# Kernel optimization log

Measured on AMD Instinct MI355X. Metric: run time of the kernel, lower is better.

Reference implementation:

```python
import jax, jax.numpy as jnp
import numpy as np

N, E, D_IN, D_H, D_OUT = 100000, 1600000, 128, 128, 16


def setup_inputs() -> dict:
    key = jax.random.key(0)
    k_x, k_e, k_w1, k_w2 = jax.random.split(key, 4)
    x = jax.random.normal(k_x, (N, D_IN), dtype=jnp.float32)
    edge_index = jax.random.randint(k_e, (2, E), 0, N, dtype=jnp.int64)
    # glorot-ish init for the two GCNConv weight matrices
    W1 = jax.random.normal(k_w1, (D_IN, D_H), dtype=jnp.float32) * (1.0 / np.sqrt(D_IN))
    b1 = jnp.zeros((D_H,), dtype=jnp.float32)
    W2 = jax.random.normal(k_w2, (D_H, D_OUT), dtype=jnp.float32) * (1.0 / np.sqrt(D_H))
    b2 = jnp.zeros((D_OUT,), dtype=jnp.float32)
    return {"x": x, "edge_index": edge_index, "W1": W1, "b1": b1, "W2": W2, "b2": b2}


def _gcn_conv(x, src, dst, norm, W, b, n):
    # linear transform, gather from source nodes, normalize, scatter-add to targets
    h = x @ W                                   # [N, d_out]
    msg = h[src] * norm[:, None]                # [E+N, d_out]
    return jax.ops.segment_sum(msg, dst, num_segments=n) + b


def reference(x, edge_index, W1, b1, W2, b2):
    n = x.shape[0]
    # GCNConv default: add self-loops, symmetric normalization D^-1/2 A D^-1/2
    loops = jnp.arange(n, dtype=edge_index.dtype)
    src = jnp.concatenate([edge_index[0], loops])
    dst = jnp.concatenate([edge_index[1], loops])
    deg = jax.ops.segment_sum(jnp.ones_like(dst, dtype=x.dtype), dst, num_segments=n)
    dinv = jnp.where(deg > 0, jax.lax.rsqrt(deg), 0.0)
    norm = dinv[src] * dinv[dst]                # [E+N]

    h = _gcn_conv(x, src, dst, norm, W1, b1, n)
    h = jax.nn.relu(h)
    # dropout is identity in eval mode (reference uses eval / deterministic path)
    out = _gcn_conv(h, src, dst, norm, W2, b2, n)
    return out
```

## Files before the change

### kernel.cpp

```cpp
#include <hip/hip_runtime.h>

typedef unsigned int uint;
typedef __attribute__((ext_vector_type(8))) short bf16x8;
typedef __attribute__((ext_vector_type(4))) float f32x4;

#define D_IN 128
#define D_H  128
#define D_OUT 16
#define NPC 512
#define NPCSH 9
#define CLDS 224
#define P1 256
#define CAP 96
#define EBCAP 12288
#define WT_STRIDE 68
#define XL_STRIDE 68

static __device__ __forceinline__ float bflo(uint u) { return __uint_as_float(u << 16); }
static __device__ __forceinline__ float bfhi(uint u) { return __uint_as_float(u & 0xFFFF0000u); }
static __device__ __forceinline__ uint f2bf(float f) {
    uint b = __float_as_uint(f);
    return (b + 0x7FFFu + ((b >> 16) & 1u)) >> 16;
}
static __device__ __forceinline__ uint pk(float a, float b) {
    return f2bf(a) | (f2bf(b) << 16);
}


__global__ __launch_bounds__(256) void k_wpack(const float* __restrict__ W1,
                                               uint* __restrict__ Wp) {
    int p = blockIdx.x * 256 + threadIdx.x;
    int k2 = p >> 7, f = p & 127;
    Wp[p] = pk(W1[(size_t)(2 * k2) * 128 + f], W1[(size_t)(2 * k2 + 1) * 128 + f]);
}


__global__ __launch_bounds__(256) void k_fill2(const int* __restrict__ src,
                                               const int* __restrict__ dst, int E, int N, int C,
                                               int chunk, int* __restrict__ cnt1,
                                               uint* __restrict__ binned1) {
    __shared__ int cur[CLDS];
    int t = threadIdx.x, b = blockIdx.x;
    for (int i = t; i < C; i += 256) cur[i] = 0;
    __syncthreads();
    int e0 = b * chunk, e1 = min(e0 + chunk, E);
    for (int e = e0 + t; e < e1; e += 256) {
        int d = dst[e];
        d = max(0, min(d, N - 1));
        int s = src[e];
        s = max(0, min(s, N - 1));
        int c = d >> NPCSH;
        int p = atomicAdd(&cur[c], 1);
        if (p < CAP) binned1[((size_t)b * C + c) * CAP + p] = ((uint)(d & (NPC - 1)) << 17) | (uint)s;
    }
    __syncthreads();
    for (int i = t; i < C; i += 256) cnt1[(size_t)i * P1 + b] = min(cur[i], CAP);
}


__global__ __launch_bounds__(256) void k_p2(const uint* __restrict__ binned1,
                                            const int* __restrict__ cnt1, int N, int C,
                                            int* __restrict__ ssrc, int* __restrict__ rowptr,
                                            int* __restrict__ deg, float* __restrict__ dinv) {
    __shared__ uint eb[EBCAP];
    __shared__ int bcnt[P1], boff[P1], ncnt[NPC], nbase_[NPC], sdata[256];
    __shared__ int total_s;
    int c = blockIdx.x, t = threadIdx.x;
    int v = cnt1[(size_t)c * P1 + t];
    bcnt[t] = v;
    sdata[t] = v;
    __syncthreads();
    for (int off = 1; off < 256; off <<= 1) {
        int xv = (t >= off) ? sdata[t - off] : 0;
        __syncthreads();
        sdata[t] += xv;
        __syncthreads();
    }
    boff[t] = sdata[t] - v;
    if (t == 255) total_s = min(sdata[255], EBCAP);
    __syncthreads();
    int total = total_s;
    int w = t >> 6, lane = t & 63;
    for (int b = w; b < P1; b += 4) {
        int n = bcnt[b], o = boff[b];
        const uint* gp = binned1 + ((size_t)b * C + c) * CAP;
        for (int j = lane; j < n; j += 64)
            if (o + j < EBCAP) eb[o + j] = gp[j];
    }
    for (int i = t; i < NPC; i += 256) ncnt[i] = 0;
    __syncthreads();
    for (int j = t; j < total; j += 256) atomicAdd(&ncnt[eb[j] >> 17], 1);
    __syncthreads();
    int v0 = ncnt[2 * t], v1 = ncnt[2 * t + 1];
    int s2 = v0 + v1;
    sdata[t] = s2;
    __syncthreads();
    for (int off = 1; off < 256; off <<= 1) {
        int xv = (t >= off) ? sdata[t - off] : 0;
        __syncthreads();
        sdata[t] += xv;
        __syncthreads();
    }
    int pre = sdata[t] - s2;
    nbase_[2 * t] = pre;
    nbase_[2 * t + 1] = pre + v0;
    __syncthreads();
    int rbase = c * EBCAP;
    for (int i = t; i < NPC; i += 256) {
        int node = c * NPC + i;
        if (node < N) {
            deg[node] = ncnt[i];
            rowptr[node] = rbase + nbase_[i];
            dinv[node] = rsqrtf((float)ncnt[i] + 1.0f);
        }
    }
    __syncthreads();
    for (int i = t; i < NPC; i += 256) ncnt[i] = nbase_[i];
    __syncthreads();
    for (int j = t; j < total; j += 256) {
        uint pe = eb[j];
        int p = atomicAdd(&ncnt[pe >> 17], 1);
        ssrc[rbase + p] = (int)(pe & 0x1FFFFu);
    }
}


__global__ __launch_bounds__(256) void k_gemm1(const float* __restrict__ x,
                                               const uint* __restrict__ Wp,
                                               const float* __restrict__ dinv, int N,
                                               uint* __restrict__ hs_b) {
    __shared__ uint Wt[128 * WT_STRIDE];
    __shared__ uint xl[128 * XL_STRIDE];
    int t = threadIdx.x;
    int row0 = blockIdx.x * 128;
    for (int p = t; p < 64 * 128; p += 256) {
        int k2 = p >> 7, f = p & 127;
        Wt[f * WT_STRIDE + k2] = Wp[p];
    }
    const float2* x2 = (const float2*)x;
    for (int p = t; p < 128 * 64; p += 256) {
        int r = p >> 6, cc = p & 63;
        int gr = row0 + r;
        float2 vv = (gr < N) ? x2[(size_t)gr * 64 + cc] : make_float2(0.f, 0.f);
        xl[r * XL_STRIDE + cc] = pk(vv.x, vv.y);
    }
    __syncthreads();
    int w = t >> 6, lane = t & 63;
    int q = lane >> 4, m = lane & 15;
    f32x4 acc[2][8];
#pragma unroll
    for (int ct = 0; ct < 2; ct++)
#pragma unroll
        for (int rt = 0; rt < 8; rt++) acc[ct][rt] = (f32x4){0.f, 0.f, 0.f, 0.f};
    for (int kc = 0; kc < 4; kc++) {
        bf16x8 afr[8];
#pragma unroll
        for (int rt = 0; rt < 8; rt++)
            afr[rt] = *(const bf16x8*)&xl[(rt * 16 + m) * XL_STRIDE + kc * 16 + q * 4];
#pragma unroll
        for (int ct = 0; ct < 2; ct++) {
            int f = w * 32 + ct * 16 + m;
            bf16x8 bfr = *(const bf16x8*)&Wt[f * WT_STRIDE + kc * 16 + q * 4];
#pragma unroll
            for (int rt = 0; rt < 8; rt++)
                acc[ct][rt] =
                    __builtin_amdgcn_mfma_f32_16x16x32_bf16(afr[rt], bfr, acc[ct][rt], 0, 0, 0);
        }
    }
    __syncthreads();
    uint* outl = xl;
#pragma unroll
    for (int rt = 0; rt < 8; rt++) {
        int gb = row0 + rt * 16 + q * 4;
        float4 dv;
        if (gb + 3 < N) {
            dv = *(const float4*)&dinv[gb];
        } else {
            dv.x = (gb < N) ? dinv[gb] : 0.f;
            dv.y = (gb + 1 < N) ? dinv[gb + 1] : 0.f;
            dv.z = (gb + 2 < N) ? dinv[gb + 2] : 0.f;
            dv.w = (gb + 3 < N) ? dinv[gb + 3] : 0.f;
        }
        float dr[4] = {dv.x, dv.y, dv.z, dv.w};
#pragma unroll
        for (int ct = 0; ct < 2; ct++) {
            f32x4 a = acc[ct][rt];
#pragma unroll
            for (int r = 0; r < 4; r++) {
                float vv = a[r] * dr[r];
                float vn = __shfl_xor(vv, 1);
                if (!(lane & 1)) {
                    int row = rt * 16 + q * 4 + r;
                    int cp = (w * 32 + ct * 16 + m) >> 1;
                    outl[row * 65 + cp] = pk(vv, vn);
                }
            }
        }
    }
    __syncthreads();
    for (int p = t; p < 128 * 64; p += 256) {
        int r = p >> 6, cc = p & 63;
        int gr = row0 + r;
        if (gr < N) hs_b[(size_t)gr * 64 + cc] = outl[r * 65 + cc];
    }
}


__global__ __launch_bounds__(256) void k_agg1(const uint* __restrict__ hs_b,
                                              const int* __restrict__ rowptr,
                                              const int* __restrict__ deg,
                                              const int* __restrict__ ssrc,
                                              const float* __restrict__ dinv,
                                              const float2* __restrict__ b1, int N,
                                              uint* __restrict__ rh_b) {
    int w = threadIdx.x >> 6, lane = threadIdx.x & 63;
    int d = blockIdx.x * 4 + w;
    if (d >= N) return;
    int start = rowptr[d], cnt = deg[d];
    uint sv = hs_b[((uint)d << 6) + lane];
    float a0 = bflo(sv), a1 = bfhi(sv);
    const int* sp = ssrc + start;
    int j = 0;
    for (; j + 8 <= cnt; j += 8) {
        int i0 = sp[j], i1 = sp[j + 1], i2 = sp[j + 2], i3 = sp[j + 3];
        int i4 = sp[j + 4], i5 = sp[j + 5], i6 = sp[j + 6], i7 = sp[j + 7];
        uint u0 = hs_b[((uint)i0 << 6) + lane];
        uint u1 = hs_b[((uint)i1 << 6) + lane];
        uint u2 = hs_b[((uint)i2 << 6) + lane];
        uint u3 = hs_b[((uint)i3 << 6) + lane];
        uint u4 = hs_b[((uint)i4 << 6) + lane];
        uint u5 = hs_b[((uint)i5 << 6) + lane];
        uint u6 = hs_b[((uint)i6 << 6) + lane];
        uint u7 = hs_b[((uint)i7 << 6) + lane];
        a0 += bflo(u0) + bflo(u1) + bflo(u2) + bflo(u3) + bflo(u4) + bflo(u5) + bflo(u6) +
              bflo(u7);
        a1 += bfhi(u0) + bfhi(u1) + bfhi(u2) + bfhi(u3) + bfhi(u4) + bfhi(u5) + bfhi(u6) +
              bfhi(u7);
    }
    for (; j < cnt; j++) {
        uint u = hs_b[((uint)sp[j] << 6) + lane];
        a0 += bflo(u);
        a1 += bfhi(u);
    }
    float sc = dinv[d];
    float2 bb = b1[lane];
    rh_b[((uint)d << 6) + lane] =
        pk(fmaxf(fmaf(a0, sc, bb.x), 0.f), fmaxf(fmaf(a1, sc, bb.y), 0.f));
}


__global__ __launch_bounds__(256) void k_gemm2(const uint* __restrict__ rh_b,
                                               const float* __restrict__ W2,
                                               const float* __restrict__ dinv, int N,
                                               uint* __restrict__ h2_b) {
    __shared__ float Wl[D_H * D_OUT];
    int t = threadIdx.x;
    for (int i = t; i < D_H * D_OUT; i += 256) Wl[i] = W2[i];
    __syncthreads();
    int r = blockIdx.x * 256 + t;
    if (r >= N) return;
    const uint* xrow = rh_b + (size_t)r * 64;
    float acc[16];
#pragma unroll
    for (int f = 0; f < 16; f++) acc[f] = 0.f;
    for (int c = 0; c < 16; c++) {
        uint4 xv = *(const uint4*)(xrow + c * 4);
        uint xs[4] = {xv.x, xv.y, xv.z, xv.w};
#pragma unroll
        for (int u = 0; u < 4; u++) {
            int k = c * 8 + u * 2;
            float x0 = bflo(xs[u]), x1 = bfhi(xs[u]);
            const float* w0 = &Wl[k * 16];
            const float* w1 = &Wl[(k + 1) * 16];
#pragma unroll
            for (int f = 0; f < 16; f++) acc[f] = fmaf(x0, w0[f], acc[f]);
#pragma unroll
            for (int f = 0; f < 16; f++) acc[f] = fmaf(x1, w1[f], acc[f]);
        }
    }
    float sc = dinv[r];
    uint o[8];
#pragma unroll
    for (int q = 0; q < 8; q++) o[q] = pk(acc[2 * q] * sc, acc[2 * q + 1] * sc);
    *(uint4*)&h2_b[(size_t)r * 8] = make_uint4(o[0], o[1], o[2], o[3]);
    *(uint4*)&h2_b[(size_t)r * 8 + 4] = make_uint4(o[4], o[5], o[6], o[7]);
}


__global__ __launch_bounds__(256) void k_agg2(const uint* __restrict__ h2_b,
                                              const int* __restrict__ rowptr,
                                              const int* __restrict__ deg,
                                              const int* __restrict__ ssrc,
                                              const float* __restrict__ dinv,
                                              const float* __restrict__ b2, int N,
                                              float2* __restrict__ out) {
    int w = threadIdx.x >> 6, lane = threadIdx.x & 63;
    int d = blockIdx.x * 4 + w;
    if (d >= N) return;
    int slot = lane >> 3, jp = lane & 7;
    int start = rowptr[d], cnt = deg[d];
    float a0 = 0.f, a1 = 0.f;
    if (slot == 0) {
        uint sv = h2_b[((uint)d << 3) + jp];
        a0 = bflo(sv);
        a1 = bfhi(sv);
    }
    const int* sp = ssrc + start;
    for (int j = slot; j < cnt; j += 8) {
        uint hv = h2_b[((uint)sp[j] << 3) + jp];
        a0 += bflo(hv);
        a1 += bfhi(hv);
    }
    a0 += __shfl_xor(a0, 8);
    a1 += __shfl_xor(a1, 8);
    a0 += __shfl_xor(a0, 16);
    a1 += __shfl_xor(a1, 16);
    a0 += __shfl_xor(a0, 32);
    a1 += __shfl_xor(a1, 32);
    if (slot == 0) {
        float di = dinv[d];
        out[(size_t)d * 8 + jp] =
            make_float2(fmaf(a0, di, b2[2 * jp]), fmaf(a1, di, b2[2 * jp + 1]));
    }
}


extern "C" void kernel_launch(void* const* d_in, const int* in_sizes, int n_in,
                              void* d_out, int out_size, void* d_ws, size_t ws_size,
                              hipStream_t stream) {
    const float* x  = (const float*)d_in[0];
    const int*   ei = (const int*)d_in[1];
    const float* W1 = (const float*)d_in[2];
    const float* b1 = (const float*)d_in[3];
    const float* W2 = (const float*)d_in[4];
    const float* b2 = (const float*)d_in[5];
    int N = in_sizes[0] / D_IN;
    int E = in_sizes[1] / 2;
    const int* src = ei;
    const int* dst = ei + E;
    int C = (N + NPC - 1) >> NPCSH;
    int chunk = (E + P1 - 1) / P1;

    char* ws = (char*)d_ws;
    size_t off = 0;
    auto alloc = [&](size_t bytes) -> char* {
        char* p = ws + off;
        off = (off + bytes + 255) & ~(size_t)255;
        return p;
    };
    uint*  Wp      = (uint*)alloc(8192 * 4);
    int*   cnt1    = (int*)alloc((size_t)P1 * C * 4);
    uint*  binned1 = (uint*)alloc((size_t)P1 * C * CAP * 4);
    int*   ssrc    = (int*)alloc((size_t)C * EBCAP * 4);
    int*   rowptr  = (int*)alloc((size_t)N * 4);
    int*   deg     = (int*)alloc((size_t)N * 4);
    float* dinv    = (float*)alloc((size_t)N * 4);
    uint*  hs_b    = (uint*)alloc((size_t)N * 64 * 4);
    uint*  rh_b    = (uint*)alloc((size_t)N * 64 * 4);
    uint*  h2_b    = hs_b;

    k_wpack<<<32, 256, 0, stream>>>(W1, Wp);
    k_fill2<<<P1, 256, 0, stream>>>(src, dst, E, N, C, chunk, cnt1, binned1);
    k_p2<<<C, 256, 0, stream>>>(binned1, cnt1, N, C, ssrc, rowptr, deg, dinv);
    k_gemm1<<<(N + 127) / 128, 256, 0, stream>>>(x, Wp, dinv, N, hs_b);
    k_agg1<<<(N + 3) / 4, 256, 0, stream>>>(hs_b, rowptr, deg, ssrc, dinv,
                                            (const float2*)b1, N, rh_b);
    k_gemm2<<<(N + 255) / 256, 256, 0, stream>>>(rh_b, W2, dinv, N, h2_b);
    k_agg2<<<(N + 3) / 4, 256, 0, stream>>>(h2_b, rowptr, deg, ssrc, dinv, b2, N,
                                            (float2*)d_out);
}
```

Before: 330.9 us.

## Slice hidden features into column slabs for cache-local layer-1 aggregation

Stores the layer-1 transformed features as 8 column slabs of 16 bf16 features each (32 bytes per node per slab), and changes the aggregation so each block handles one slab. Within a wave, eight edges are gathered in parallel and combined with a shuffle reduction. Keeping each slab at about 3.2 MB is meant to let random neighbor gathers stay in L2/MALL instead of hitting HBM. It also folds the weight-pack kernel into the edge-binning kernel to save a launch. In exchange, the aggregation grid is eight times larger, index lists are re-read once per slab, and each gather is only 32 bytes.

```diff
diff --git a/kernel.cpp b/kernel.cpp
--- a/kernel.cpp
+++ b/kernel.cpp
@@ -27,20 +27,19 @@
 }
 
 
-__global__ __launch_bounds__(256) void k_wpack(const float* __restrict__ W1,
-                                               uint* __restrict__ Wp) {
-    int p = blockIdx.x * 256 + threadIdx.x;
-    int k2 = p >> 7, f = p & 127;
-    Wp[p] = pk(W1[(size_t)(2 * k2) * 128 + f], W1[(size_t)(2 * k2 + 1) * 128 + f]);
-}
-
-
 __global__ __launch_bounds__(256) void k_fill2(const int* __restrict__ src,
                                                const int* __restrict__ dst, int E, int N, int C,
                                                int chunk, int* __restrict__ cnt1,
-                                               uint* __restrict__ binned1) {
+                                               uint* __restrict__ binned1,
+                                               const float* __restrict__ W1,
+                                               uint* __restrict__ Wp) {
     __shared__ int cur[CLDS];
     int t = threadIdx.x, b = blockIdx.x;
+    if (b < 32) {
+        int p = b * 256 + t;
+        int k2 = p >> 7, f = p & 127;
+        Wp[p] = pk(W1[(size_t)(2 * k2) * 128 + f], W1[(size_t)(2 * k2 + 1) * 128 + f]);
+    }
     for (int i = t; i < C; i += 256) cur[i] = 0;
     __syncthreads();
     int e0 = b * chunk, e1 = min(e0 + chunk, E);
@@ -127,8 +126,8 @@
 
 __global__ __launch_bounds__(256) void k_gemm1(const float* __restrict__ x,
                                                const uint* __restrict__ Wp,
-                                               const float* __restrict__ dinv, int N,
-                                               uint* __restrict__ hs_b) {
+                                               const float* __restrict__ dinv, int N, int SL,
+                                               uint* __restrict__ hs_s) {
     __shared__ uint Wt[128 * WT_STRIDE];
     __shared__ uint xl[128 * XL_STRIDE];
     int t = threadIdx.x;
@@ -198,60 +197,63 @@
         }
     }
     __syncthreads();
-    for (int p = t; p < 128 * 64; p += 256) {
-        int r = p >> 6, cc = p & 63;
-        int gr = row0 + r;
-        if (gr < N) hs_b[(size_t)gr * 64 + cc] = outl[r * 65 + cc];
-    }
-}
-
-
-__global__ __launch_bounds__(256) void k_agg1(const uint* __restrict__ hs_b,
+    for (int i = t; i < 128 * 64; i += 256) {
+        int s = i >> 10, rr = (i >> 3) & 127, u = i & 7;
+        int gr = row0 + rr;
+        if (gr < N) hs_s[(size_t)s * SL + ((size_t)gr << 3) + u] = outl[rr * 65 + s * 8 + u];
+    }
+}
+
+
+__global__ __launch_bounds__(256) void k_agg1(const uint* __restrict__ hs_s,
                                               const int* __restrict__ rowptr,
                                               const int* __restrict__ deg,
                                               const int* __restrict__ ssrc,
                                               const float* __restrict__ dinv,
-                                              const float2* __restrict__ b1, int N,
-                                              uint* __restrict__ rh_b) {
+                                              const float2* __restrict__ b1, int N, int SL,
+                                              uint* __restrict__ rh_s) {
     int w = threadIdx.x >> 6, lane = threadIdx.x & 63;
-    int d = blockIdx.x * 4 + w;
+    int bid = blockIdx.x;
+    int s = bid & 7;
+    int d = (bid >> 3) * 4 + w;
     if (d >= N) return;
+    const uint* hb = hs_s + (size_t)s * SL;
+    int slot = lane >> 3, u = lane & 7;
     int start = rowptr[d], cnt = deg[d];
-    uint sv = hs_b[((uint)d << 6) + lane];
-    float a0 = bflo(sv), a1 = bfhi(sv);
     const int* sp = ssrc + start;
-    int j = 0;
-    for (; j + 8 <= cnt; j += 8) {
-        int i0 = sp[j], i1 = sp[j + 1], i2 = sp[j + 2], i3 = sp[j + 3];
-        int i4 = sp[j + 4], i5 = sp[j + 5], i6 = sp[j + 6], i7 = sp[j + 7];
-        uint u0 = hs_b[((uint)i0 << 6) + lane];
-        uint u1 = hs_b[((uint)i1 << 6) + lane];
-        uint u2 = hs_b[((uint)i2 << 6) + lane];
-        uint u3 = hs_b[((uint)i3 << 6) + lane];
-        uint u4 = hs_b[((uint)i4 << 6) + lane];
-        uint u5 = hs_b[((uint)i5 << 6) + lane];
-        uint u6 = hs_b[((uint)i6 << 6) + lane];
-        uint u7 = hs_b[((uint)i7 << 6) + lane];
-        a0 += bflo(u0) + bflo(u1) + bflo(u2) + bflo(u3) + bflo(u4) + bflo(u5) + bflo(u6) +
-              bflo(u7);
-        a1 += bfhi(u0) + bfhi(u1) + bfhi(u2) + bfhi(u3) + bfhi(u4) + bfhi(u5) + bfhi(u6) +
-              bfhi(u7);
-    }
-    for (; j < cnt; j++) {
-        uint u = hs_b[((uint)sp[j] << 6) + lane];
-        a0 += bflo(u);
-        a1 += bfhi(u);
-    }
-    float sc = dinv[d];
-    float2 bb = b1[lane];
-    rh_b[((uint)d << 6) + lane] =
-        pk(fmaxf(fmaf(a0, sc, bb.x), 0.f), fmaxf(fmaf(a1, sc, bb.y), 0.f));
-}
-
-
-__global__ __launch_bounds__(256) void k_gemm2(const uint* __restrict__ rh_b,
+    float a0 = 0.f, a1 = 0.f;
+    int j = slot;
+    for (; j + 8 < cnt; j += 16) {
+        uint v0 = hb[((uint)sp[j] << 3) + u];
+        uint v1 = hb[((uint)sp[j + 8] << 3) + u];
+        a0 += bflo(v0) + bflo(v1);
+        a1 += bfhi(v0) + bfhi(v1);
+    }
+    for (; j < cnt; j += 8) {
+        uint v = hb[((uint)sp[j] << 3) + u];
+        a0 += bflo(v);
+        a1 += bfhi(v);
+    }
+    a0 += __shfl_xor(a0, 8);
+    a1 += __shfl_xor(a1, 8);
+    a0 += __shfl_xor(a0, 16);
+    a1 += __shfl_xor(a1, 16);
+    a0 += __shfl_xor(a0, 32);
+    a1 += __shfl_xor(a1, 32);
+    if (slot == 0) {
+        uint sv = hb[((uint)d << 3) + u];
+        float di = dinv[d];
+        float2 bb = b1[s * 8 + u];
+        float r0 = fmaxf(fmaf(a0 + bflo(sv), di, bb.x), 0.f);
+        float r1 = fmaxf(fmaf(a1 + bfhi(sv), di, bb.y), 0.f);
+        rh_s[(size_t)s * SL + ((uint)d << 3) + u] = pk(r0, r1);
+    }
+}
+
+
+__global__ __launch_bounds__(256) void k_gemm2(const uint* __restrict__ rh_s,
                                                const float* __restrict__ W2,
-                                               const float* __restrict__ dinv, int N,
+                                               const float* __restrict__ dinv, int N, int SL,
                                                uint* __restrict__ h2_b) {
     __shared__ float Wl[D_H * D_OUT];
     int t = threadIdx.x;
@@ -259,16 +261,17 @@
     __syncthreads();
     int r = blockIdx.x * 256 + t;
     if (r >= N) return;
-    const uint* xrow = rh_b + (size_t)r * 64;
     float acc[16];
 #pragma unroll
     for (int f = 0; f < 16; f++) acc[f] = 0.f;
-    for (int c = 0; c < 16; c++) {
-        uint4 xv = *(const uint4*)(xrow + c * 4);
-        uint xs[4] = {xv.x, xv.y, xv.z, xv.w};
-#pragma unroll
-        for (int u = 0; u < 4; u++) {
-            int k = c * 8 + u * 2;
+    for (int s = 0; s < 8; s++) {
+        const uint* xp = rh_s + (size_t)s * SL + ((size_t)r << 3);
+        uint4 xa = *(const uint4*)xp;
+        uint4 xb = *(const uint4*)(xp + 4);
+        uint xs[8] = {xa.x, xa.y, xa.z, xa.w, xb.x, xb.y, xb.z, xb.w};
+#pragma unroll
+        for (int u = 0; u < 8; u++) {
+            int k = s * 16 + u * 2;
             float x0 = bflo(xs[u]), x1 = bfhi(xs[u]);
             const float* w0 = &Wl[k * 16];
             const float* w1 = &Wl[(k + 1) * 16];
@@ -340,6 +343,7 @@
     const int* dst = ei + E;
     int C = (N + NPC - 1) >> NPCSH;
     int chunk = (E + P1 - 1) / P1;
+    int SL = N * 8;
 
     char* ws = (char*)d_ws;
     size_t off = 0;
@@ -355,17 +359,16 @@
     int*   rowptr  = (int*)alloc((size_t)N * 4);
     int*   deg     = (int*)alloc((size_t)N * 4);
     float* dinv    = (float*)alloc((size_t)N * 4);
-    uint*  hs_b    = (uint*)alloc((size_t)N * 64 * 4);
-    uint*  rh_b    = (uint*)alloc((size_t)N * 64 * 4);
-    uint*  h2_b    = hs_b;
-
-    k_wpack<<<32, 256, 0, stream>>>(W1, Wp);
-    k_fill2<<<P1, 256, 0, stream>>>(src, dst, E, N, C, chunk, cnt1, binned1);
+    uint*  hs_s    = (uint*)alloc((size_t)N * 64 * 4);
+    uint*  rh_s    = (uint*)alloc((size_t)N * 64 * 4);
+    uint*  h2_b    = hs_s;
+
+    k_fill2<<<P1, 256, 0, stream>>>(src, dst, E, N, C, chunk, cnt1, binned1, W1, Wp);
     k_p2<<<C, 256, 0, stream>>>(binned1, cnt1, N, C, ssrc, rowptr, deg, dinv);
-    k_gemm1<<<(N + 127) / 128, 256, 0, stream>>>(x, Wp, dinv, N, hs_b);
-    k_agg1<<<(N + 3) / 4, 256, 0, stream>>>(hs_b, rowptr, deg, ssrc, dinv,
-                                            (const float2*)b1, N, rh_b);
-    k_gemm2<<<(N + 255) / 256, 256, 0, stream>>>(rh_b, W2, dinv, N, h2_b);
+    k_gemm1<<<(N + 127) / 128, 256, 0, stream>>>(x, Wp, dinv, N, SL, hs_s);
+    k_agg1<<<((N + 3) / 4) * 8, 256, 0, stream>>>(hs_s, rowptr, deg, ssrc, dinv,
+                                                  (const float2*)b1, N, SL, rh_s);
+    k_gemm2<<<(N + 255) / 256, 256, 0, stream>>>(rh_s, W2, dinv, N, SL, h2_b);
     k_agg2<<<(N + 3) / 4, 256, 0, stream>>>(h2_b, rowptr, deg, ssrc, dinv, b2, N,
                                             (float2*)d_out);
 }
```

Measured after the change: 461.9 us. +39.6%, slower.
